# Kernel tuning notes

Measured on AMD Instinct MI355X. Metric: run time of the kernel, lower is better.

## Reference

```python
import jax, jax.numpy as jnp
import numpy as np
from jax import lax

EPS = 1e-5  # torch BatchNorm2d default


def setup_inputs() -> dict:
    key = jax.random.key(0)
    k1, k2, k3 = jax.random.split(key, 3)
    C = 64
    x = jax.random.normal(k1, (32, C, 128, 128), dtype=jnp.float32)
    # per-channel 3x3 depthwise weights (OIHW with I=1, feature_group_count=C)
    w = jax.random.normal(k2, (C, 1, 3, 3), dtype=jnp.float32) * (1.0 / 3.0)
    b = jax.random.normal(k3, (C,), dtype=jnp.float32) * 0.1
    gamma = jnp.ones((C,), dtype=jnp.float32)
    beta = jnp.zeros((C,), dtype=jnp.float32)
    return {"x": x, "w": w, "b": b, "gamma": gamma, "beta": beta}


def reference(x, w, b, gamma, beta):
    C = x.shape[1]
    # depthwise 3x3 conv, stride 1, padding 1 (same math as C separate Conv2d(1,1,3))
    y = lax.conv_general_dilated(
        x, w,
        window_strides=(1, 1),
        padding=((1, 1), (1, 1)),
        feature_group_count=C,
        dimension_numbers=("NCHW", "OIHW", "NCHW"),
    )
    y = y + b[None, :, None, None]
    # BatchNorm2d(1) per channel in training mode: batch stats over (N, H, W),
    # biased variance, eps=1e-5
    mean = jnp.mean(y, axis=(0, 2, 3), keepdims=True)
    var = jnp.var(y, axis=(0, 2, 3), keepdims=True)
    y_hat = (y - mean) * lax.rsqrt(var + EPS)
    out = y_hat * gamma[None, :, None, None] + beta[None, :, None, None]
    return jax.nn.relu(out)
```

## Files before the change

### kernel.cpp

```cpp
#include <hip/hip_runtime.h>

#define HW        128
#define PLANE     16384
#define NCH       64
#define NB        32
#define NQ        4
#define NPART     8192
#define COUNT_INV (1.0f / 524288.0f)
#define EPSV      1e-5f

typedef float f4v __attribute__((ext_vector_type(4)));


__device__ __forceinline__ void load_win(const float* __restrict__ bp, int r0, int w4,
                                         bool hasL, bool hasR, float (&v)[6][6]) {
#pragma unroll
    for (int i = 0; i < 6; ++i) {
        int g = r0 - 1 + i;
        if ((unsigned)g < (unsigned)HW) {
            const float* rp = bp + g * HW + w4;
            float4 m = *(const float4*)rp;
            v[i][0] = hasL ? rp[-1] : 0.f;
            v[i][1] = m.x; v[i][2] = m.y; v[i][3] = m.z; v[i][4] = m.w;
            v[i][5] = hasR ? rp[4] : 0.f;
        } else {
#pragma unroll
            for (int j = 0; j < 6; ++j) v[i][j] = 0.f;
        }
    }
}

__device__ __forceinline__ void conv_row(const float (&tp)[6], const float (&md)[6],
                                         const float (&bt)[6], const float* W,
                                         float bias, float (&acc)[4]) {
#pragma unroll
    for (int j = 0; j < 4; ++j) {
        float a = bias;
        a = fmaf(tp[j],     W[0], a);
        a = fmaf(tp[j + 1], W[1], a);
        a = fmaf(tp[j + 2], W[2], a);
        a = fmaf(md[j],     W[3], a);
        a = fmaf(md[j + 1], W[4], a);
        a = fmaf(md[j + 2], W[5], a);
        a = fmaf(bt[j],     W[6], a);
        a = fmaf(bt[j + 1], W[7], a);
        a = fmaf(bt[j + 2], W[8], a);
        acc[j] = a;
    }
}

__global__ __launch_bounds__(256) void pass_stats(const float* __restrict__ x,
                                                  const float* __restrict__ wgt,
                                                  const float* __restrict__ bias,
                                                  float* __restrict__ partials) {
    __shared__ float red[8];
    const int bid   = blockIdx.x;
    const int q     = bid & 3;
    const int plane = bid >> 2;
    const int c     = plane & 63;
    const int n     = plane >> 6;
    const int t     = threadIdx.x;
    const int cg    = t & 31, rg = t >> 5;
    const int w4    = cg * 4, r0 = q * 32 + rg * 4;
    const bool hasL = (cg != 0), hasR = (cg != 31);

    float W[9];
#pragma unroll
    for (int k = 0; k < 9; ++k) W[k] = wgt[c * 9 + k];
    const float bv = bias[c];
    const float* bp = x + (size_t)plane * PLANE;

    float v[6][6];
    load_win(bp, r0, w4, hasL, hasR, v);

    float sum = 0.f, sq = 0.f;
#pragma unroll
    for (int k = 0; k < 4; ++k) {
        float acc[4];
        conv_row(v[k], v[k + 1], v[k + 2], W, bv, acc);
#pragma unroll
        for (int j = 0; j < 4; ++j) {
            sum += acc[j];
            sq = fmaf(acc[j], acc[j], sq);
        }
    }

#pragma unroll
    for (int off = 32; off; off >>= 1) {
        sum += __shfl_down(sum, off);
        sq  += __shfl_down(sq, off);
    }
    const int wave = t >> 6, lane = t & 63;
    if (lane == 0) { red[wave] = sum; red[4 + wave] = sq; }
    __syncthreads();
    if (t == 0) {
        const int pi = n * 4 + q;
        partials[c * 128 + pi]         = red[0] + red[1] + red[2] + red[3];
        partials[NPART + c * 128 + pi] = red[4] + red[5] + red[6] + red[7];
    }
}

__global__ __launch_bounds__(256) void pass_apply(const float* __restrict__ x,
                                                  const float* __restrict__ wgt,
                                                  const float* __restrict__ bias,
                                                  const float* __restrict__ partials,
                                                  const float* __restrict__ gamma,
                                                  const float* __restrict__ beta,
                                                  float* __restrict__ out) {
    const int bid   = blockIdx.x;
    const int q     = bid & 3;
    const int plane = bid >> 2;
    const int c     = plane & 63;
    const int t     = threadIdx.x;
    const int cg    = t & 31, rg = t >> 5;
    const int w4    = cg * 4, r0 = q * 32 + rg * 4;
    const bool hasL = (cg != 0), hasR = (cg != 31);

    float W[9];
#pragma unroll
    for (int k = 0; k < 9; ++k) W[k] = wgt[c * 9 + k];
    const float bv = bias[c];
    const float* bp = x + (size_t)plane * PLANE;

    float v[6][6];
    load_win(bp, r0, w4, hasL, hasR, v);

    const int lane = t & 63;
    float S = partials[c * 128 + lane]         + partials[c * 128 + 64 + lane];
    float Q = partials[NPART + c * 128 + lane] + partials[NPART + c * 128 + 64 + lane];
#pragma unroll
    for (int off = 32; off; off >>= 1) {
        S += __shfl_xor(S, off);
        Q += __shfl_xor(Q, off);
    }
    const float mean = S * COUNT_INV;
    const float var  = fmaxf(Q * COUNT_INV - mean * mean, 0.f);
    const float s    = gamma[c] * rsqrtf(var + EPSV);
    const float sh   = fmaf(bv, s, beta[c] - mean * s);

    float* op = out + (size_t)plane * PLANE;
#pragma unroll
    for (int k = 0; k < 4; ++k) {
        float acc[4];
        conv_row(v[k], v[k + 1], v[k + 2], W, 0.f, acc);
        f4v o;
        o.x = fmaxf(fmaf(acc[0], s, sh), 0.f);
        o.y = fmaxf(fmaf(acc[1], s, sh), 0.f);
        o.z = fmaxf(fmaf(acc[2], s, sh), 0.f);
        o.w = fmaxf(fmaf(acc[3], s, sh), 0.f);
        __builtin_nontemporal_store(o, (f4v*)(op + (r0 + k) * HW + w4));
    }
}

extern "C" void kernel_launch(void* const* d_in, const int* in_sizes, int n_in,
                              void* d_out, int out_size, void* d_ws, size_t ws_size,
                              hipStream_t stream) {
    const float* x     = (const float*)d_in[0];
    const float* w     = (const float*)d_in[1];
    const float* b     = (const float*)d_in[2];
    const float* gamma = (const float*)d_in[3];
    const float* beta  = (const float*)d_in[4];
    float* out = (float*)d_out;
    float* ws  = (float*)d_ws;

    pass_stats<<<NB * NCH * NQ, 256, 0, stream>>>(x, w, b, ws);
    pass_apply<<<NB * NCH * NQ, 256, 0, stream>>>(x, w, b, ws, gamma, beta, out);
}
```

Baseline: 75.02 us.

## Materialize conv output in fp16 workspace instead of recomputing conv in apply pass

The stats pass now also writes the depthwise conv result (with bias) as fp16 into the workspace, and the second pass reads that fp16 tensor and applies the normalization and ReLU instead of re-reading x and recomputing the convolution. This removes the redundant conv and halo reads in the second pass but adds an fp16 write and read round trip. Storing the intermediate in fp16 reduces precision of the output. The original two-pass path is kept as a fallback when the workspace is too small.

```diff
diff --git a/kernel.cpp b/kernel.cpp
--- a/kernel.cpp
+++ b/kernel.cpp
@@ -9,7 +9,12 @@
 #define COUNT_INV (1.0f / 524288.0f)
 #define EPSV      1e-5f
 
-typedef float f4v __attribute__((ext_vector_type(4)));
+#define YELEMS    (NB * NCH * PLANE)
+#define PART_OFF  (YELEMS / 2)
+#define WS_NEED   ((size_t)YELEMS * 2 + 16384 * 4)
+
+typedef float    f4v __attribute__((ext_vector_type(4)));
+typedef _Float16 h4v __attribute__((ext_vector_type(4)));
 
 
 __device__ __forceinline__ void load_win(const float* __restrict__ bp, int r0, int w4,
@@ -49,10 +54,11 @@
     }
 }
 
-__global__ __launch_bounds__(256) void pass_stats(const float* __restrict__ x,
-                                                  const float* __restrict__ wgt,
-                                                  const float* __restrict__ bias,
-                                                  float* __restrict__ partials) {
+__global__ __launch_bounds__(256) void pass_conv_stats(const float* __restrict__ x,
+                                                       const float* __restrict__ wgt,
+                                                       const float* __restrict__ bias,
+                                                       _Float16* __restrict__ yh,
+                                                       float* __restrict__ partials) {
     __shared__ float red[8];
     const int bid   = blockIdx.x;
     const int q     = bid & 3;
@@ -69,6 +75,7 @@
     for (int k = 0; k < 9; ++k) W[k] = wgt[c * 9 + k];
     const float bv = bias[c];
     const float* bp = x + (size_t)plane * PLANE;
+    _Float16* yp = yh + (size_t)plane * PLANE;
 
     float v[6][6];
     load_win(bp, r0, w4, hasL, hasR, v);
@@ -78,6 +85,10 @@
     for (int k = 0; k < 4; ++k) {
         float acc[4];
         conv_row(v[k], v[k + 1], v[k + 2], W, bv, acc);
+        h4v hv;
+        hv.x = (_Float16)acc[0]; hv.y = (_Float16)acc[1];
+        hv.z = (_Float16)acc[2]; hv.w = (_Float16)acc[3];
+        *(h4v*)(yp + (r0 + k) * HW + w4) = hv;
 #pragma unroll
         for (int j = 0; j < 4; ++j) {
             sum += acc[j];
@@ -100,13 +111,105 @@
     }
 }
 
-__global__ __launch_bounds__(256) void pass_apply(const float* __restrict__ x,
-                                                  const float* __restrict__ wgt,
-                                                  const float* __restrict__ bias,
-                                                  const float* __restrict__ partials,
-                                                  const float* __restrict__ gamma,
-                                                  const float* __restrict__ beta,
-                                                  float* __restrict__ out) {
+__global__ __launch_bounds__(256) void pass_norm(const _Float16* __restrict__ yh,
+                                                 const float* __restrict__ partials,
+                                                 const float* __restrict__ gamma,
+                                                 const float* __restrict__ beta,
+                                                 float* __restrict__ out) {
+    const int bid   = blockIdx.x;
+    const int q     = bid & 3;
+    const int plane = bid >> 2;
+    const int c     = plane & 63;
+    const int t     = threadIdx.x;
+    const int cg    = t & 31, rg = t >> 5;
+    const int w4    = cg * 4, r0 = q * 32 + rg * 4;
+
+    const _Float16* yp = yh + (size_t)plane * PLANE;
+
+    h4v hv[4];
+#pragma unroll
+    for (int k = 0; k < 4; ++k)
+        hv[k] = *(const h4v*)(yp + (r0 + k) * HW + w4);
+
+    const int lane = t & 63;
+    float S = partials[c * 128 + lane]         + partials[c * 128 + 64 + lane];
+    float Q = partials[NPART + c * 128 + lane] + partials[NPART + c * 128 + 64 + lane];
+#pragma unroll
+    for (int off = 32; off; off >>= 1) {
+        S += __shfl_xor(S, off);
+        Q += __shfl_xor(Q, off);
+    }
+    const float mean = S * COUNT_INV;
+    const float var  = fmaxf(Q * COUNT_INV - mean * mean, 0.f);
+    const float s    = gamma[c] * rsqrtf(var + EPSV);
+    const float sh   = beta[c] - mean * s;
+
+    float* op = out + (size_t)plane * PLANE;
+#pragma unroll
+    for (int k = 0; k < 4; ++k) {
+        f4v o;
+        o.x = fmaxf(fmaf((float)hv[k].x, s, sh), 0.f);
+        o.y = fmaxf(fmaf((float)hv[k].y, s, sh), 0.f);
+        o.z = fmaxf(fmaf((float)hv[k].z, s, sh), 0.f);
+        o.w = fmaxf(fmaf((float)hv[k].w, s, sh), 0.f);
+        __builtin_nontemporal_store(o, (f4v*)(op + (r0 + k) * HW + w4));
+    }
+}
+
+__global__ __launch_bounds__(256) void pass_stats_fb(const float* __restrict__ x,
+                                                     const float* __restrict__ wgt,
+                                                     const float* __restrict__ bias,
+                                                     float* __restrict__ partials) {
+    __shared__ float red[8];
+    const int bid   = blockIdx.x;
+    const int q     = bid & 3;
+    const int plane = bid >> 2;
+    const int c     = plane & 63;
+    const int n     = plane >> 6;
+    const int t     = threadIdx.x;
+    const int cg    = t & 31, rg = t >> 5;
+    const int w4    = cg * 4, r0 = q * 32 + rg * 4;
+    const bool hasL = (cg != 0), hasR = (cg != 31);
+
+    float W[9];
+#pragma unroll
+    for (int k = 0; k < 9; ++k) W[k] = wgt[c * 9 + k];
+    const float bv = bias[c];
+    const float* bp = x + (size_t)plane * PLANE;
+
+    float v[6][6];
+    load_win(bp, r0, w4, hasL, hasR, v);
+
+    float sum = 0.f, sq = 0.f;
+#pragma unroll
+    for (int k = 0; k < 4; ++k) {
+        float acc[4];
+        conv_row(v[k], v[k + 1], v[k + 2], W, bv, acc);
+#pragma unroll
+        for (int j = 0; j < 4; ++j) { sum += acc[j]; sq = fmaf(acc[j], acc[j], sq); }
+    }
+#pragma unroll
+    for (int off = 32; off; off >>= 1) {
+        sum += __shfl_down(sum, off);
+        sq  += __shfl_down(sq, off);
+    }
+    const int wave = t >> 6, lane = t & 63;
+    if (lane == 0) { red[wave] = sum; red[4 + wave] = sq; }
+    __syncthreads();
+    if (t == 0) {
+        const int pi = n * 4 + q;
+        partials[c * 128 + pi]         = red[0] + red[1] + red[2] + red[3];
+        partials[NPART + c * 128 + pi] = red[4] + red[5] + red[6] + red[7];
+    }
+}
+
+__global__ __launch_bounds__(256) void pass_apply_fb(const float* __restrict__ x,
+                                                     const float* __restrict__ wgt,
+                                                     const float* __restrict__ bias,
+                                                     const float* __restrict__ partials,
+                                                     const float* __restrict__ gamma,
+                                                     const float* __restrict__ beta,
+                                                     float* __restrict__ out) {
     const int bid   = blockIdx.x;
     const int q     = bid & 3;
     const int plane = bid >> 2;
@@ -161,8 +264,15 @@
     const float* gamma = (const float*)d_in[3];
     const float* beta  = (const float*)d_in[4];
     float* out = (float*)d_out;
-    float* ws  = (float*)d_ws;
-
-    pass_stats<<<NB * NCH * NQ, 256, 0, stream>>>(x, w, b, ws);
-    pass_apply<<<NB * NCH * NQ, 256, 0, stream>>>(x, w, b, ws, gamma, beta, out);
-}
+
+    if (ws_size >= WS_NEED) {
+        _Float16* yh  = (_Float16*)d_ws;
+        float* parts  = (float*)d_ws + PART_OFF;
+        pass_conv_stats<<<NB * NCH * NQ, 256, 0, stream>>>(x, w, b, yh, parts);
+        pass_norm<<<NB * NCH * NQ, 256, 0, stream>>>(yh, parts, gamma, beta, out);
+    } else {
+        float* parts = (float*)d_ws;
+        pass_stats_fb<<<NB * NCH * NQ, 256, 0, stream>>>(x, w, b, parts);
+        pass_apply_fb<<<NB * NCH * NQ, 256, 0, stream>>>(x, w, b, parts, gamma, beta, out);
+    }
+}
```

Result: faster. 73.04 us (-2.6%).

## Materialize conv output in fp16 workspace and simplify normalize pass

Applied to the files above, without the earlier changes.

The first pass now writes the depthwise conv result, including bias, as fp16 into the workspace while it computes the batch statistics. The second pass reads this fp16 intermediate and applies the affine normalisation and ReLU, so it no longer re-reads x and recomputes the convolution. It also uses one block per plane with 8x8 tiles per thread. Total DRAM bytes stay about the same, and the fp16 intermediate adds rounding error to the output.

```diff
diff --git a/kernel.cpp b/kernel.cpp
--- a/kernel.cpp
+++ b/kernel.cpp
@@ -9,7 +9,13 @@
 #define COUNT_INV (1.0f / 524288.0f)
 #define EPSV      1e-5f
 
-typedef float f4v __attribute__((ext_vector_type(4)));
+#define YELEMS    (NB * NCH * PLANE)
+#define PART_OFF  (YELEMS / 2)
+#define WS_NEED   ((size_t)YELEMS * 2 + 16384 * 4)
+
+typedef float    f4v __attribute__((ext_vector_type(4)));
+typedef _Float16 h4v __attribute__((ext_vector_type(4)));
+typedef _Float16 h8v __attribute__((ext_vector_type(8)));
 
 
 __device__ __forceinline__ void load_win(const float* __restrict__ bp, int r0, int w4,
@@ -49,10 +55,11 @@
     }
 }
 
-__global__ __launch_bounds__(256) void pass_stats(const float* __restrict__ x,
-                                                  const float* __restrict__ wgt,
-                                                  const float* __restrict__ bias,
-                                                  float* __restrict__ partials) {
+__global__ __launch_bounds__(256) void pass_conv_stats(const float* __restrict__ x,
+                                                       const float* __restrict__ wgt,
+                                                       const float* __restrict__ bias,
+                                                       _Float16* __restrict__ yh,
+                                                       float* __restrict__ partials) {
     __shared__ float red[8];
     const int bid   = blockIdx.x;
     const int q     = bid & 3;
@@ -69,6 +76,7 @@
     for (int k = 0; k < 9; ++k) W[k] = wgt[c * 9 + k];
     const float bv = bias[c];
     const float* bp = x + (size_t)plane * PLANE;
+    _Float16* yp = yh + (size_t)plane * PLANE;
 
     float v[6][6];
     load_win(bp, r0, w4, hasL, hasR, v);
@@ -78,6 +86,10 @@
     for (int k = 0; k < 4; ++k) {
         float acc[4];
         conv_row(v[k], v[k + 1], v[k + 2], W, bv, acc);
+        h4v hv;
+        hv.x = (_Float16)acc[0]; hv.y = (_Float16)acc[1];
+        hv.z = (_Float16)acc[2]; hv.w = (_Float16)acc[3];
+        *(h4v*)(yp + (r0 + k) * HW + w4) = hv;
 #pragma unroll
         for (int j = 0; j < 4; ++j) {
             sum += acc[j];
@@ -100,30 +112,23 @@
     }
 }
 
-__global__ __launch_bounds__(256) void pass_apply(const float* __restrict__ x,
-                                                  const float* __restrict__ wgt,
-                                                  const float* __restrict__ bias,
-                                                  const float* __restrict__ partials,
-                                                  const float* __restrict__ gamma,
-                                                  const float* __restrict__ beta,
-                                                  float* __restrict__ out) {
-    const int bid   = blockIdx.x;
-    const int q     = bid & 3;
-    const int plane = bid >> 2;
+__global__ __launch_bounds__(256) void pass_norm(const _Float16* __restrict__ yh,
+                                                 const float* __restrict__ partials,
+                                                 const float* __restrict__ gamma,
+                                                 const float* __restrict__ beta,
+                                                 float* __restrict__ out) {
+    const int plane = blockIdx.x;
     const int c     = plane & 63;
     const int t     = threadIdx.x;
-    const int cg    = t & 31, rg = t >> 5;
-    const int w4    = cg * 4, r0 = q * 32 + rg * 4;
-    const bool hasL = (cg != 0), hasR = (cg != 31);
+    const int cgrp  = t & 15, rgrp = t >> 4;
+    const int col0  = cgrp * 8, row0 = rgrp * 8;
 
-    float W[9];
+    const _Float16* yp = yh + (size_t)plane * PLANE;
+
+    h8v hv[8];
 #pragma unroll
-    for (int k = 0; k < 9; ++k) W[k] = wgt[c * 9 + k];
-    const float bv = bias[c];
-    const float* bp = x + (size_t)plane * PLANE;
-
-    float v[6][6];
-    load_win(bp, r0, w4, hasL, hasR, v);
+    for (int r = 0; r < 8; ++r)
+        hv[r] = __builtin_nontemporal_load((const h8v*)(yp + (row0 + r) * HW + col0));
 
     const int lane = t & 63;
     float S = partials[c * 128 + lane]         + partials[c * 128 + 64 + lane];
@@ -136,19 +141,23 @@
     const float mean = S * COUNT_INV;
     const float var  = fmaxf(Q * COUNT_INV - mean * mean, 0.f);
     const float s    = gamma[c] * rsqrtf(var + EPSV);
-    const float sh   = fmaf(bv, s, beta[c] - mean * s);
+    const float sh   = beta[c] - mean * s;
 
     float* op = out + (size_t)plane * PLANE;
 #pragma unroll
-    for (int k = 0; k < 4; ++k) {
-        float acc[4];
-        conv_row(v[k], v[k + 1], v[k + 2], W, 0.f, acc);
-        f4v o;
-        o.x = fmaxf(fmaf(acc[0], s, sh), 0.f);
-        o.y = fmaxf(fmaf(acc[1], s, sh), 0.f);
-        o.z = fmaxf(fmaf(acc[2], s, sh), 0.f);
-        o.w = fmaxf(fmaf(acc[3], s, sh), 0.f);
-        __builtin_nontemporal_store(o, (f4v*)(op + (r0 + k) * HW + w4));
+    for (int r = 0; r < 8; ++r) {
+        f4v o0, o1;
+        o0.x = fmaxf(fmaf((float)hv[r][0], s, sh), 0.f);
+        o0.y = fmaxf(fmaf((float)hv[r][1], s, sh), 0.f);
+        o0.z = fmaxf(fmaf((float)hv[r][2], s, sh), 0.f);
+        o0.w = fmaxf(fmaf((float)hv[r][3], s, sh), 0.f);
+        o1.x = fmaxf(fmaf((float)hv[r][4], s, sh), 0.f);
+        o1.y = fmaxf(fmaf((float)hv[r][5], s, sh), 0.f);
+        o1.z = fmaxf(fmaf((float)hv[r][6], s, sh), 0.f);
+        o1.w = fmaxf(fmaf((float)hv[r][7], s, sh), 0.f);
+        float* rp = op + (row0 + r) * HW + col0;
+        __builtin_nontemporal_store(o0, (f4v*)rp);
+        __builtin_nontemporal_store(o1, (f4v*)(rp + 4));
     }
 }
 
@@ -161,8 +170,9 @@
     const float* gamma = (const float*)d_in[3];
     const float* beta  = (const float*)d_in[4];
     float* out = (float*)d_out;
-    float* ws  = (float*)d_ws;
 
-    pass_stats<<<NB * NCH * NQ, 256, 0, stream>>>(x, w, b, ws);
-    pass_apply<<<NB * NCH * NQ, 256, 0, stream>>>(x, w, b, ws, gamma, beta, out);
+    _Float16* yh  = (_Float16*)d_ws;
+    float* parts  = (float*)d_ws + PART_OFF;
+    pass_conv_stats<<<NB * NCH * NQ, 256, 0, stream>>>(x, w, b, yh, parts);
+    pass_norm<<<NB * NCH, 256, 0, stream>>>(yh, parts, gamma, beta, out);
 }
```

After: 115.1 us. +53.4%, slower.
